# Performance work log

Measured on AMD Instinct MI355X. Metric: run time of the kernel, lower is better.

The kernel has to match this reference:

```python
import jax, jax.numpy as jnp
import numpy as np

S_DIM, T_DIM, FEAT_DIM = 2048, 2048, 128
NCE_N, NCE_T, NCE_MOM = 16384, 0.07, 0.5
N_DATA, BATCH = 100000, 64
EPS = 1e-7


def _l2norm(x):
    return x / jnp.linalg.norm(x, axis=1, keepdims=True)


def setup_inputs() -> dict:
    key = jax.random.key(0)
    ks = jax.random.split(key, 10)
    feat_s = jax.random.normal(ks[0], (BATCH, S_DIM), dtype=jnp.float32)
    feat_t = jax.random.normal(ks[1], (BATCH, T_DIM), dtype=jnp.float32)
    idx = jax.random.randint(ks[2], (BATCH,), 0, N_DATA)
    sample_idx = jax.random.randint(ks[3], (BATCH, NCE_N + 1), 0, N_DATA)
    sample_idx = sample_idx.at[:, 0].set(idx)  # positive sample in column 0
    # Embed linear weights (Linear(dim_in, feat_dim))
    w_s = jax.random.normal(ks[4], (FEAT_DIM, S_DIM), dtype=jnp.float32) / np.sqrt(S_DIM)
    b_s = jnp.zeros((FEAT_DIM,), dtype=jnp.float32)
    w_t = jax.random.normal(ks[5], (FEAT_DIM, T_DIM), dtype=jnp.float32) / np.sqrt(T_DIM)
    b_t = jnp.zeros((FEAT_DIM,), dtype=jnp.float32)
    # memory banks, uniform(-stdv, stdv), stdv = 1/sqrt(feat_dim/3)
    stdv = 1.0 / np.sqrt(FEAT_DIM / 3.0)
    mem_v1 = jax.random.uniform(ks[6], (N_DATA, FEAT_DIM), dtype=jnp.float32, minval=-stdv, maxval=stdv)
    mem_v2 = jax.random.uniform(ks[7], (N_DATA, FEAT_DIM), dtype=jnp.float32, minval=-stdv, maxval=stdv)
    return {"feat_s": feat_s, "feat_t": feat_t, "idx": idx, "sample_idx": sample_idx,
            "w_s": w_s, "b_s": b_s, "w_t": w_t, "b_t": b_t,
            "mem_v1": mem_v1, "mem_v2": mem_v2}


def _contrast_out(mem, samp_idx, v):
    # gather [B, K+1, D] from memory bank, bmm against [B, D]
    w = mem[samp_idx]                                # [B, K+1, D]
    logits = jnp.einsum('bkd,bd->bk', w, v) / NCE_T  # [B, K+1]
    out = jnp.exp(logits)
    z = jnp.mean(out) * N_DATA                       # first-pass Z estimate
    return out / z


def _contrast_loss(x):
    b = x.shape[0]
    m = float(NCE_N) / N_DATA
    log_d1 = jnp.log(x[:, 0] / (x[:, 0] + m + EPS))          # positives
    log_d0 = jnp.log(m / (x[:, 1:] + m + EPS))               # negatives
    return -(jnp.sum(log_d1) + jnp.sum(log_d0)) / b


def reference(feat_s, feat_t, idx, sample_idx, w_s, b_s, w_t, b_t, mem_v1, mem_v2):
    hs = _l2norm(feat_s @ w_s.T + b_s)  # [B, D]
    ht = _l2norm(feat_t @ w_t.T + b_t)  # [B, D]
    out_s = _contrast_out(mem_v2, sample_idx, hs)  # anchor=student vs teacher memory
    out_t = _contrast_out(mem_v1, sample_idx, ht)  # anchor=teacher vs student memory
    return _contrast_loss(out_s) + _contrast_loss(out_t)
```

## Files before the change

kernel.cpp:

```cpp
#include <hip/hip_runtime.h>

#define DIM_IN   2048
#define FEAT     128
#define KP1      16385
#define NDATA    100000
#define BATCH    64
#define NB       128
#define NBLK     ((NDATA + NB - 1) / NB)
#define GCH      16

constexpr float NCE_T_INV = 1.0f / 0.07f;
constexpr float M_CONST   = 16384.0f / 100000.0f;
constexpr float EPS_C     = 1e-7f;

typedef short bf16x8 __attribute__((ext_vector_type(8)));
typedef float f32x4  __attribute__((ext_vector_type(4)));

#define VP_PLANE 34816
#define VP_SIDE  17408
#define VP_ROW   272

__global__ void __launch_bounds__(1024) embed_kernel(
    const float* __restrict__ feat_s, const float* __restrict__ feat_t,
    const float* __restrict__ w_s, const float* __restrict__ b_s,
    const float* __restrict__ w_t, const float* __restrict__ b_t,
    char* __restrict__ vplanes, float* __restrict__ z_zero,
    float* __restrict__ out_zero)
{
    const int blk  = blockIdx.x;
    const int side = blk >> 6;
    const int b    = blk & 63;
    const float* feat = (side == 0 ? feat_s : feat_t) + (size_t)b * DIM_IN;
    const float* w    = (side == 0 ? w_s : w_t);
    const float* bias = (side == 0 ? b_s : b_t);

    __shared__ float sfeat[DIM_IN];
    __shared__ float pre[FEAT];
    __shared__ float wsum[2];

    const int t = threadIdx.x;
    if (blk == 0) {
        if (t < 128) z_zero[t] = 0.f;
        else if (t == 128) out_zero[0] = 0.f;
    }
    {
        const float4* f4 = (const float4*)feat;
        float4* s4 = (float4*)sfeat;
        if (t < 512) s4[t] = f4[t];
    }
    __syncthreads();

    const int wv = t >> 6, ln = t & 63;
    const float4* w4  = (const float4*)w;
    const float4* sf4 = (const float4*)sfeat;
#pragma unroll 2
    for (int i = 0; i < 8; ++i) {
        const int d = wv + i * 16;
        float s = 0.f;
#pragma unroll
        for (int seg = 0; seg < 8; ++seg) {
            float4 a = w4[d * (DIM_IN / 4) + seg * 64 + ln];
            float4 f = sf4[seg * 64 + ln];
            s += a.x * f.x + a.y * f.y + a.z * f.z + a.w * f.w;
        }
#pragma unroll
        for (int o = 32; o > 0; o >>= 1) s += __shfl_xor(s, o, 64);
        if (ln == 0) pre[d] = s;
    }
    __syncthreads();

    if (t < 128) {
        float p = pre[t] + bias[t];
        pre[t] = p;
        float sq = p * p;
#pragma unroll
        for (int o = 32; o > 0; o >>= 1) sq += __shfl_xor(sq, o, 64);
        if ((t & 63) == 0) wsum[t >> 6] = sq;
    }
    __syncthreads();
    if (t < 128) {
        float inv_norm = 1.0f / sqrtf(wsum[0] + wsum[1]);
        float x = pre[t] * inv_norm;
        unsigned int u = __float_as_uint(x);
        unsigned short h = (unsigned short)(u >> 16);
        float hf = __uint_as_float(u & 0xffff0000u);
        float lr = x - hf;
        unsigned short l = (unsigned short)(__float_as_uint(lr) >> 16);
        const size_t off = (size_t)side * VP_SIDE + (size_t)b * VP_ROW + t * 2;
        *(unsigned short*)(vplanes + off)            = h;
        *(unsigned short*)(vplanes + VP_PLANE + off) = l;
    }
}

__global__ void __launch_bounds__(512) gemm_exp_kernel(
    const float* __restrict__ mem_v1, const float* __restrict__ mem_v2,
    const char* __restrict__ vplanes, float* __restrict__ E)
{
    __shared__ __align__(16) char lds[75776];

    const int bx   = blockIdx.x;
    const int side = bx & 1;
    const int tile = bx >> 1;
    const int n0   = tile * NB;
    const float* bank = (side == 0 ? mem_v2 : mem_v1);
    const int t  = threadIdx.x;
    const int wv = t >> 6, ln = t & 63;
    const int lm = ln & 15;
    const int kb = ln >> 4;

    {
        const char* hbase = vplanes + (size_t)side * VP_SIDE;
        const char* lbase = vplanes + VP_PLANE + (size_t)side * VP_SIDE;
        for (int seg = wv; seg < 34; seg += 8) {
            const char* src = (seg < 17 ? hbase + seg * 1024
                                        : lbase + (seg - 17) * 1024) + ln * 16;
            __builtin_amdgcn_global_load_lds(
                (const __attribute__((address_space(1))) void*)src,
                (__attribute__((address_space(3))) void*)(lds + seg * 1024),
                16, 0, 0);
        }
    }

    const int r = t >> 2;
    const int q = t & 3;
    int rowg = n0 + r; if (rowg > NDATA - 1) rowg = NDATA - 1;
    const float* bsrc = bank + (size_t)rowg * FEAT;

    f32x4 acc[4];
#pragma unroll
    for (int mi = 0; mi < 4; ++mi) acc[mi] = (f32x4){0.f, 0.f, 0.f, 0.f};

    float4 sa, sb;
    {
        const float4* p = (const float4*)(bsrc + 0 * 32 + q * 8);
        sa = p[0]; sb = p[1];
    }
    {
        float xs[8] = {sa.x, sa.y, sa.z, sa.w, sb.x, sb.y, sb.z, sb.w};
        bf16x8 H, L;
#pragma unroll
        for (int j = 0; j < 8; ++j) {
            unsigned int u = __float_as_uint(xs[j]);
            H[j] = (short)(u >> 16);
            float hf = __uint_as_float(u & 0xffff0000u);
            L[j] = (short)(__float_as_uint(xs[j] - hf) >> 16);
        }
        char* base = lds + 34816;
        *(bf16x8*)(base + r * 80 + q * 16) = H;
        *(bf16x8*)(base + 10240 + r * 80 + q * 16) = L;
    }
    __syncthreads();

    const int nloc = wv * 16 + lm;

#pragma unroll 1
    for (int c = 0; c < 4; ++c) {
        float4 na, nb;
        if (c < 3) {
            const float4* p = (const float4*)(bsrc + (c + 1) * 32 + q * 8);
            na = p[0]; nb = p[1];
        }
        bf16x8 ah[4], al[4];
#pragma unroll
        for (int mi = 0; mi < 4; ++mi) {
            ah[mi] = *(const bf16x8*)(lds + (mi * 16 + lm) * VP_ROW + c * 64 + kb * 16);
            al[mi] = *(const bf16x8*)(lds + 17408 + (mi * 16 + lm) * VP_ROW + c * 64 + kb * 16);
        }
        const char* bb = lds + 34816 + (c & 1) * 20480;
        bf16x8 bh = *(const bf16x8*)(bb + nloc * 80 + kb * 16);
        bf16x8 bl = *(const bf16x8*)(bb + 10240 + nloc * 80 + kb * 16);

#pragma unroll
        for (int mi = 0; mi < 4; ++mi) {
            acc[mi] = __builtin_amdgcn_mfma_f32_16x16x32_bf16(ah[mi], bh, acc[mi], 0, 0, 0);
            acc[mi] = __builtin_amdgcn_mfma_f32_16x16x32_bf16(al[mi], bh, acc[mi], 0, 0, 0);
            acc[mi] = __builtin_amdgcn_mfma_f32_16x16x32_bf16(ah[mi], bl, acc[mi], 0, 0, 0);
        }

        if (c < 3) {
            float xs[8] = {na.x, na.y, na.z, na.w, nb.x, nb.y, nb.z, nb.w};
            bf16x8 H, L;
#pragma unroll
            for (int j = 0; j < 8; ++j) {
                unsigned int u = __float_as_uint(xs[j]);
                H[j] = (short)(u >> 16);
                float hf = __uint_as_float(u & 0xffff0000u);
                L[j] = (short)(__float_as_uint(xs[j] - hf) >> 16);
            }
            char* base = lds + 34816 + ((c + 1) & 1) * 20480;
            *(bf16x8*)(base + r * 80 + q * 16) = H;
            *(bf16x8*)(base + 10240 + r * 80 + q * 16) = L;
        }
        __syncthreads();
    }

    const int nn = n0 + nloc;
    if (nn < NDATA) {
#pragma unroll
        for (int mi = 0; mi < 4; ++mi)
#pragma unroll
            for (int j = 0; j < 4; ++j) {
                const int anchor = mi * 16 + kb * 4 + j;
                E[(size_t)(side * 64 + anchor) * NDATA + nn] =
                    __expf(acc[mi][j] * NCE_T_INV);
            }
    }
}

__global__ void __launch_bounds__(256) gather_z_kernel(
    const int* __restrict__ sample_idx, const float* __restrict__ E,
    float* __restrict__ ex_out, float* __restrict__ z_out)
{
    const int blk   = blockIdx.x;
    const int chunk = blk >> 7;
    const int sb    = blk & 127;
    const int b     = sb & 63;
    const float* Eb = E + (size_t)sb * NDATA;

    float zp = 0.f;
    for (int k = chunk * 256 + threadIdx.x; k < KP1; k += GCH * 256) {
        const int idx = sample_idx[(size_t)b * KP1 + k];
        const float e = Eb[idx];
        ex_out[(size_t)sb * KP1 + k] = e;
        zp += e;
    }
#pragma unroll
    for (int o = 32; o > 0; o >>= 1) zp += __shfl_xor(zp, o, 64);
    __shared__ float zw[4];
    if ((threadIdx.x & 63) == 0) zw[threadIdx.x >> 6] = zp;
    __syncthreads();
    if (threadIdx.x == 0) atomicAdd(&z_out[sb], zw[0] + zw[1] + zw[2] + zw[3]);
}

__global__ void __launch_bounds__(256) loss_kernel(
    const float* __restrict__ ex_in, const float* __restrict__ z_in,
    float* __restrict__ out)
{
    const int blk   = blockIdx.x;
    const int chunk = blk >> 7;
    const int sb    = blk & 127;
    const int side  = sb >> 6;

    __shared__ float zsh;
    if (threadIdx.x < 64) {
        float zv = z_in[side * 64 + threadIdx.x];
#pragma unroll
        for (int o = 32; o > 0; o >>= 1) zv += __shfl_xor(zv, o, 64);
        if (threadIdx.x == 0) zsh = zv;
    }
    __syncthreads();

    const float z  = zsh * ((float)NDATA / (64.0f * (float)KP1));
    const float rz = 1.0f / z;
    const float* ex = ex_in + (size_t)sb * KP1;

    float part = 0.f;
    for (int k = chunk * 256 + threadIdx.x; k < KP1; k += 512) {
        const float x = ex[k] * rz;
        if (k == 0) part += __logf(x / (x + M_CONST + EPS_C));
        else        part += __logf(M_CONST / (x + M_CONST + EPS_C));
    }
#pragma unroll
    for (int o = 32; o > 0; o >>= 1) part += __shfl_xor(part, o, 64);
    __shared__ float pw[4];
    if ((threadIdx.x & 63) == 0) pw[threadIdx.x >> 6] = part;
    __syncthreads();
    if (threadIdx.x == 0)
        atomicAdd(out, -(pw[0] + pw[1] + pw[2] + pw[3]) * (1.0f / 64.0f));
}

extern "C" void kernel_launch(void* const* d_in, const int* in_sizes, int n_in,
                              void* d_out, int out_size, void* d_ws, size_t ws_size,
                              hipStream_t stream)
{
    const float* feat_s     = (const float*)d_in[0];
    const float* feat_t     = (const float*)d_in[1];
    const int*   sample_idx = (const int*)  d_in[3];
    const float* w_s        = (const float*)d_in[4];
    const float* b_s        = (const float*)d_in[5];
    const float* w_t        = (const float*)d_in[6];
    const float* b_t        = (const float*)d_in[7];
    const float* mem_v1     = (const float*)d_in[8];
    const float* mem_v2     = (const float*)d_in[9];
    float* out = (float*)d_out;

    char*  ws     = (char*)d_ws;
    float* ws_z   = (float*)ws;
    float* ws_ex  = (float*)(ws + 512);
    char*  ws_vp  = (char*)(ws + 512);
    float* ws_E   = (float*)(ws + 512 + (size_t)2 * BATCH * KP1 * sizeof(float));

    embed_kernel<<<2 * BATCH, 1024, 0, stream>>>(feat_s, feat_t, w_s, b_s, w_t, b_t,
                                                 ws_vp, ws_z, out);
    gemm_exp_kernel<<<2 * NBLK, 512, 0, stream>>>(mem_v1, mem_v2, ws_vp, ws_E);
    gather_z_kernel<<<2 * BATCH * GCH, 256, 0, stream>>>(sample_idx, ws_E, ws_ex, ws_z);
    loss_kernel<<<2 * BATCH * 2, 256, 0, stream>>>(ws_ex, ws_z, out);
}
```

Measured before the change: 204.7 us.

## Load memory-bank B operand directly into registers in MFMA layout, drop LDS staging

Each lane now loads its own bank row slice straight from global memory into registers, already in the MFMA B-fragment layout. All four K-chunks are issued up front, before the vplanes LDS copy. This removes the B-operand LDS double buffer, the per-chunk syncthreads and the LDS round trip, and cuts shared memory from about 74KB to 34KB, which may allow more resident blocks. In exchange, register use rises (8 float4 per thread), and the global reads become per-lane 32-byte accesses across rows instead of the previous cooperative pattern, which could reduce coalescing.

```diff
diff --git a/kernel.cpp b/kernel.cpp
--- a/kernel.cpp
+++ b/kernel.cpp
@@ -96,7 +96,7 @@
     const float* __restrict__ mem_v1, const float* __restrict__ mem_v2,
     const char* __restrict__ vplanes, float* __restrict__ E)
 {
-    __shared__ __align__(16) char lds[75776];
+    __shared__ __align__(16) char lds[34816];
 
     const int bx   = blockIdx.x;
     const int side = bx & 1;
@@ -107,6 +107,17 @@
     const int wv = t >> 6, ln = t & 63;
     const int lm = ln & 15;
     const int kb = ln >> 4;
+    const int nloc = wv * 16 + lm;
+
+    int rowg = n0 + nloc; if (rowg > NDATA - 1) rowg = NDATA - 1;
+    const float* bsrc = bank + (size_t)rowg * FEAT;
+    float4 bq[8];
+#pragma unroll
+    for (int c = 0; c < 4; ++c) {
+        const float4* p = (const float4*)(bsrc + c * 32 + kb * 8);
+        bq[c * 2 + 0] = p[0];
+        bq[c * 2 + 1] = p[1];
+    }
 
     {
         const char* hbase = vplanes + (size_t)side * VP_SIDE;
@@ -121,44 +132,23 @@
         }
     }
 
-    const int r = t >> 2;
-    const int q = t & 3;
-    int rowg = n0 + r; if (rowg > NDATA - 1) rowg = NDATA - 1;
-    const float* bsrc = bank + (size_t)rowg * FEAT;
-
     f32x4 acc[4];
 #pragma unroll
     for (int mi = 0; mi < 4; ++mi) acc[mi] = (f32x4){0.f, 0.f, 0.f, 0.f};
 
-    float4 sa, sb;
-    {
-        const float4* p = (const float4*)(bsrc + 0 * 32 + q * 8);
-        sa = p[0]; sb = p[1];
-    }
-    {
-        float xs[8] = {sa.x, sa.y, sa.z, sa.w, sb.x, sb.y, sb.z, sb.w};
-        bf16x8 H, L;
+    __syncthreads();
+
+#pragma unroll
+    for (int c = 0; c < 4; ++c) {
+        const float xs[8] = {bq[c*2].x,   bq[c*2].y,   bq[c*2].z,   bq[c*2].w,
+                             bq[c*2+1].x, bq[c*2+1].y, bq[c*2+1].z, bq[c*2+1].w};
+        bf16x8 bh, bl;
 #pragma unroll
         for (int j = 0; j < 8; ++j) {
             unsigned int u = __float_as_uint(xs[j]);
-            H[j] = (short)(u >> 16);
+            bh[j] = (short)(u >> 16);
             float hf = __uint_as_float(u & 0xffff0000u);
-            L[j] = (short)(__float_as_uint(xs[j] - hf) >> 16);
-        }
-        char* base = lds + 34816;
-        *(bf16x8*)(base + r * 80 + q * 16) = H;
-        *(bf16x8*)(base + 10240 + r * 80 + q * 16) = L;
-    }
-    __syncthreads();
-
-    const int nloc = wv * 16 + lm;
-
-#pragma unroll 1
-    for (int c = 0; c < 4; ++c) {
-        float4 na, nb;
-        if (c < 3) {
-            const float4* p = (const float4*)(bsrc + (c + 1) * 32 + q * 8);
-            na = p[0]; nb = p[1];
+            bl[j] = (short)(__float_as_uint(xs[j] - hf) >> 16);
         }
         bf16x8 ah[4], al[4];
 #pragma unroll
@@ -166,32 +156,12 @@
             ah[mi] = *(const bf16x8*)(lds + (mi * 16 + lm) * VP_ROW + c * 64 + kb * 16);
             al[mi] = *(const bf16x8*)(lds + 17408 + (mi * 16 + lm) * VP_ROW + c * 64 + kb * 16);
         }
-        const char* bb = lds + 34816 + (c & 1) * 20480;
-        bf16x8 bh = *(const bf16x8*)(bb + nloc * 80 + kb * 16);
-        bf16x8 bl = *(const bf16x8*)(bb + 10240 + nloc * 80 + kb * 16);
-
 #pragma unroll
         for (int mi = 0; mi < 4; ++mi) {
             acc[mi] = __builtin_amdgcn_mfma_f32_16x16x32_bf16(ah[mi], bh, acc[mi], 0, 0, 0);
             acc[mi] = __builtin_amdgcn_mfma_f32_16x16x32_bf16(al[mi], bh, acc[mi], 0, 0, 0);
             acc[mi] = __builtin_amdgcn_mfma_f32_16x16x32_bf16(ah[mi], bl, acc[mi], 0, 0, 0);
         }
-
-        if (c < 3) {
-            float xs[8] = {na.x, na.y, na.z, na.w, nb.x, nb.y, nb.z, nb.w};
-            bf16x8 H, L;
-#pragma unroll
-            for (int j = 0; j < 8; ++j) {
-                unsigned int u = __float_as_uint(xs[j]);
-                H[j] = (short)(u >> 16);
-                float hf = __uint_as_float(u & 0xffff0000u);
-                L[j] = (short)(__float_as_uint(xs[j] - hf) >> 16);
-            }
-            char* base = lds + 34816 + ((c + 1) & 1) * 20480;
-            *(bf16x8*)(base + r * 80 + q * 16) = H;
-            *(bf16x8*)(base + 10240 + r * 80 + q * 16) = L;
-        }
-        __syncthreads();
     }
 
     const int nn = n0 + nloc;
```

New measurement: 204.2 us. No clear change (-0.2%).
